# Kernel tuning notes

Measured on AMD Instinct MI355X. Metric: run time of the kernel, lower is better.

Reference implementation:

```python
import jax, jax.numpy as jnp
import numpy as np

K = 3
PAD = 1

def conv2d(x, w, b=None):
    # x: [B,C,H,W], w: [O,C,kh,kw], stride 1, padding 1
    y = jax.lax.conv_general_dilated(x, w, (1, 1), [(PAD, PAD), (PAD, PAD)],
                                     dimension_numbers=('NCHW', 'OIHW', 'NCHW'))
    if b is not None:
        y = y + b[None, :, None, None]
    return y

def deform_conv2d(x, offset, mask, w):
    # Faithful torchvision DeformConv2d (v2, stride=1, dilation=1, pad=1, no bias).
    # x: [B,C,H,W]; offset: [B,2*K*K,H,W] with (dy,dx) interleaved per kernel pt;
    # mask: [B,K*K,H,W]; w: [O,C,K,K]
    B, C, H, W = x.shape
    KK = K * K
    off = offset.reshape(B, KK, 2, H, W)
    offs_y, offs_x = off[:, :, 0], off[:, :, 1]           # [B,KK,H,W]
    ky = (jnp.arange(KK) // K).astype(jnp.float32) - PAD   # kernel row offsets
    kx = (jnp.arange(KK) % K).astype(jnp.float32) - PAD    # kernel col offsets
    py = offs_y + jnp.arange(H, dtype=jnp.float32)[None, None, :, None] + ky[None, :, None, None]
    px = offs_x + jnp.arange(W, dtype=jnp.float32)[None, None, None, :] + kx[None, :, None, None]
    y0f = jnp.floor(py); x0f = jnp.floor(px)
    wy = py - y0f; wx = px - x0f                           # bilinear fractions
    y0 = y0f.astype(jnp.int32); x0 = x0f.astype(jnp.int32)
    xf = x.reshape(B, C, H * W)

    def corner(yi, xi):
        valid = ((yi >= 0) & (yi < H) & (xi >= 0) & (xi < W)).astype(x.dtype)
        idx = jnp.clip(yi, 0, H - 1) * W + jnp.clip(xi, 0, W - 1)   # [B,KK,H,W]
        g = jax.vmap(lambda img, ix: img[:, ix])(xf, idx.reshape(B, KK * H * W))
        return g.reshape(B, C, KK, H, W) * valid[:, None]

    one = jnp.asarray(1.0, x.dtype)
    samp = (corner(y0, x0)         * ((one - wy) * (one - wx))[:, None]
          + corner(y0, x0 + 1)     * ((one - wy) * wx)[:, None]
          + corner(y0 + 1, x0)     * (wy * (one - wx))[:, None]
          + corner(y0 + 1, x0 + 1) * (wy * wx)[:, None])       # [B,C,KK,H,W]
    if mask is not None:
        samp = samp * mask[:, None]
    O = w.shape[0]
    return jnp.einsum('bckhw,ock->bohw', samp, w.reshape(O, C, KK))

def setup_inputs() -> dict:
    key = jax.random.key(0)
    ks = jax.random.split(key, 7)
    B, C, O, H, W = 4, 64, 64, 128, 128
    x = jax.random.normal(ks[0], (B, C, H, W), jnp.float32)
    ele = jax.random.normal(ks[1], (B, 1, H, W), jnp.float32)
    offset_w = jax.random.normal(ks[2], (2 * K * K, 1, 3, 3), jnp.float32) * 0.1
    offset_b = jnp.zeros((2 * K * K,), jnp.float32)
    mask_w = jax.random.normal(ks[3], (K * K, C, 3, 3), jnp.float32) * (1.0 / np.sqrt(C * 9))
    mask_b = jnp.zeros((K * K,), jnp.float32)
    deform_w = jax.random.normal(ks[4], (O, C, K, K), jnp.float32) * (1.0 / np.sqrt(C * 9))
    return {"x": x, "ele": ele, "offset_w": offset_w, "offset_b": offset_b,
            "mask_w": mask_w, "mask_b": mask_b, "deform_w": deform_w}

def reference(x, ele, offset_w, offset_b, mask_w, mask_b, deform_w):
    offset = conv2d(ele, offset_w, offset_b)                 # [B,18,H,W]
    mask = jax.nn.sigmoid(conv2d(x, mask_w, mask_b))         # [B,9,H,W]
    out = deform_conv2d(x, offset, mask, deform_w)           # [B,O,H,W]
    return jax.nn.relu(out)
```

## Files before the change

kernel.cpp:

```cpp
#include <hip/hip_runtime.h>
#include <hip/hip_bf16.h>
#include <hip/hip_fp16.h>

typedef _Float16 half8 __attribute__((ext_vector_type(8)));
typedef _Float16 half2v __attribute__((ext_vector_type(2)));
typedef float f32x4 __attribute__((ext_vector_type(4)));

#define B_ 4
#define C_ 64
#define O_ 64
#define H_ 128
#define W_ 128
#define HT 8
#define WT 16
#define HALO 3
#define RS 14
#define CS 22

__device__ __forceinline__ unsigned pkh(float lo, float hi) {
  half2v v = {(_Float16)lo, (_Float16)hi};
  return __builtin_bit_cast(unsigned, v);
}

__global__ void build_frags(const float* __restrict__ dw,
                            const float* __restrict__ mw,
                            _Float16* __restrict__ wsb) {
  int t = blockIdx.x * 256 + threadIdx.x;
  if (t < 36864) {
    int j = t & 7, lane = (t >> 3) & 63, ot = (t >> 9) & 3, s = t >> 11;
    int kk = s >> 1, ch = s & 1;
    int o = ot * 16 + (lane & 15);
    int c = ch * 32 + ((lane >> 4) << 3) + j;
    wsb[t] = (_Float16)dw[(o * 64 + c) * 9 + kk];
  } else if (t < 46080) {
    int t2 = t - 36864;
    int j = t2 & 7, lane = (t2 >> 3) & 63, s = t2 >> 9;
    int km = lane & 15;
    int c = (s & 1) * 32 + ((lane >> 4) << 3) + j;
    int tap = s >> 1;
    float v = (km < 9) ? mw[(km * 64 + c) * 9 + tap] : 0.0f;
    wsb[t] = (_Float16)v;
  }
}

__global__ __launch_bounds__(512, 4)
void deform_main(const float* __restrict__ x,
                 const float* __restrict__ ele,
                 const float* __restrict__ ow,
                 const float* __restrict__ ob,
                 const float* __restrict__ mb,
                 const _Float16* __restrict__ wsb,
                 float* __restrict__ out) {
  __shared__ uint4 xs4[RS * CS * 9];
  __shared__ _Float16 offl[128 * 18];
  __shared__ uint2 cwb[128 * 9];
  __shared__ unsigned crc[128 * 9];

  const int tid = threadIdx.x;
  const int lane = tid & 63;
  const int wv = tid >> 6;
  const int pcl = lane & 15;
  const int lq = lane >> 4;

  const int bid = blockIdx.x;
  const int d = ((bid & 7) << 6) + (bid >> 3);
  const int b = d >> 7;
  const int t7 = d & 127;
  const int r0 = (t7 >> 3) * HT;
  const int c0 = (t7 & 7) * WT;

  float ev[9];
  {
    int tl = tid & 127;
    int pr = tl >> 4, pc = tl & 15;
    int h = r0 + pr, w = c0 + pc;
#pragma unroll
    for (int ty = 0; ty < 3; ++ty)
#pragma unroll
      for (int tx = 0; tx < 3; ++tx) {
        int gy = h - 1 + ty, gx = w - 1 + tx;
        float v = 0.0f;
        if ((unsigned)gy < 128u && (unsigned)gx < 128u)
          v = ele[b * (H_ * W_) + (gy << 7) + gx];
        ev[ty * 3 + tx] = v;
      }
  }

  {
    _Float16* xsb = (_Float16*)xs4;
    const int c2 = tid >> 4;
    const int pl = tid & 15;
    const float* xb0 = x + b * (C_ * H_ * W_) + (2 * c2) * (H_ * W_);
    const float* xb1 = xb0 + (H_ * W_);
    for (int p = pl; p < RS * CS; p += 16) {
      int row = (p * 2979) >> 16;
      int col = p - row * CS;
      int gy = r0 - HALO + row, gx = c0 - HALO + col;
      float v0 = 0.0f, v1 = 0.0f;
      if ((unsigned)gy < 128u && (unsigned)gx < 128u) {
        int gi = (gy << 7) + gx;
        v0 = xb0[gi];
        v1 = xb1[gi];
      }
      half2v hv = {(_Float16)v0, (_Float16)v1};
      *(half2v*)&xsb[p * 72 + 2 * c2] = hv;
    }
  }

  if (tid < 128) {
#pragma unroll
    for (int ci = 0; ci < 18; ++ci) {
      float a = ob[ci];
#pragma unroll
      for (int tap = 0; tap < 9; ++tap) a += ev[tap] * ow[ci * 9 + tap];
      offl[tid * 18 + ci] = (_Float16)a;
    }
  }
  __syncthreads();

  {
    const half8* wfm8 = ((const half8*)wsb) + 4608;
    f32x4 macc = {0.f, 0.f, 0.f, 0.f};
#pragma unroll
    for (int s = 0; s < 18; ++s) {
      const int tap = s >> 1;
      const int chalf = s & 1;
      const int ty = tap / 3, tx = tap - ty * 3;
      half8 aw = wfm8[s * 64 + lane];
      const int csl = chalf * 4 + lq;
      int rc = (wv + (HALO - 1) + ty) * CS + (pcl + (HALO - 1) + tx);
      half8 xv = *(const half8*)(xs4 + rc * 9 + csl);
      macc = __builtin_amdgcn_mfma_f32_16x16x32_f16(aw, xv, macc, 0, 0, 0);
    }
    const int px = wv * 16 + pcl;
    const int h = r0 + wv, w = c0 + pcl;
#pragma unroll
    for (int r = 0; r < 4; ++r) {
      int kk = lq * 4 + r;
      if (kk < 9) {
        float a = macc[r] + mb[kk];
        float m = 1.0f / (1.0f + __expf(-a));
        int ky = kk / 3 - 1;
        int kx = kk - (kk / 3) * 3 - 1;
        half2v o2 = *(const half2v*)&offl[px * 18 + kk * 2];
        float py = (float)(h + ky) + (float)o2[0];
        float pxx = (float)(w + kx) + (float)o2[1];
        float fy = floorf(py), fx = floorf(pxx);
        float wy = py - fy, wx = pxx - fx;
        int iy = (int)fy - r0 + HALO;
        int ix = (int)fx - c0 + HALO;
        int vy0 = (unsigned)iy < (unsigned)RS;
        int vy1 = (unsigned)(iy + 1) < (unsigned)RS;
        int vx0 = (unsigned)ix < (unsigned)CS;
        int vx1 = (unsigned)(ix + 1) < (unsigned)CS;
        int cy0 = min(max(iy, 0), RS - 1), cy1 = min(max(iy + 1, 0), RS - 1);
        int cx0 = min(max(ix, 0), CS - 1), cx1 = min(max(ix + 1, 0), CS - 1);
        float wy0 = 1.0f - wy, wx0 = 1.0f - wx;
        float a00 = wy0 * wx0 * m * (float)(vy0 & vx0);
        float a01 = wy0 * wx * m * (float)(vy0 & vx1);
        float a10 = wy * wx0 * m * (float)(vy1 & vx0);
        float a11 = wy * wx * m * (float)(vy1 & vx1);
        int rc00 = cy0 * CS + cx0;
        int drow = (cy1 - cy0) * CS;
        int dcol = cx1 - cx0;
        uint2 cv;
        cv.x = pkh(a00, a01);
        cv.y = pkh(a10, a11);
        cwb[px * 9 + kk] = cv;
        crc[px * 9 + kk] =
            (unsigned)rc00 | ((unsigned)drow << 16) | ((unsigned)dcol << 24);
      }
    }
  }
  __syncthreads();

  const half8* wf8 = (const half8*)wsb;
  f32x4 acc[4];
#pragma unroll
  for (int ot = 0; ot < 4; ++ot) {
    f32x4 z = {0.f, 0.f, 0.f, 0.f};
    acc[ot] = z;
  }

  const int px = wv * 16 + pcl;

#pragma unroll
  for (int kk = 0; kk < 9; ++kk) {
    uint2 cv = cwb[px * 9 + kk];
    unsigned rv = crc[px * 9 + kk];
    int rc00 = rv & 0xFFFF;
    int drow = (rv >> 16) & 0xFF;
    int dcol = rv >> 24;
    int rc01 = rc00 + dcol;
    int rc10 = rc00 + drow;
    int rc11 = rc10 + dcol;
    half2v c01 = __builtin_bit_cast(half2v, cv.x);
    half2v c23 = __builtin_bit_cast(half2v, cv.y);
    _Float16 a00 = c01[0], a01 = c01[1], a10 = c23[0], a11 = c23[1];
    half8 a00s = {a00, a00, a00, a00, a00, a00, a00, a00};
    half8 a01s = {a01, a01, a01, a01, a01, a01, a01, a01};
    half8 a10s = {a10, a10, a10, a10, a10, a10, a10, a10};
    half8 a11s = {a11, a11, a11, a11, a11, a11, a11, a11};
#pragma unroll
    for (int ch = 0; ch < 2; ++ch) {
      const int csl = ch * 4 + lq;
      half8 v00 = *(const half8*)(xs4 + rc00 * 9 + csl);
      half8 v01 = *(const half8*)(xs4 + rc01 * 9 + csl);
      half8 v10 = *(const half8*)(xs4 + rc10 * 9 + csl);
      half8 v11 = *(const half8*)(xs4 + rc11 * 9 + csl);
      half8 t = v00 * a00s + v01 * a01s + v10 * a10s + v11 * a11s;
      const int sidx = kk * 2 + ch;
#pragma unroll
      for (int ot = 0; ot < 4; ++ot) {
        half8 bw = wf8[(sidx * 4 + ot) * 64 + lane];
        acc[ot] = __builtin_amdgcn_mfma_f32_16x16x32_f16(bw, t, acc[ot], 0, 0, 0);
      }
    }
  }

  const int h = r0 + wv;
  const int w = c0 + pcl;
#pragma unroll
  for (int ot = 0; ot < 4; ++ot) {
#pragma unroll
    for (int r = 0; r < 4; ++r) {
      int o = ot * 16 + lq * 4 + r;
      float v = fmaxf(acc[ot][r], 0.0f);
      out[((b * O_ + o) << 14) + (h << 7) + w] = v;
    }
  }
}

extern "C" void kernel_launch(void* const* d_in, const int* in_sizes, int n_in,
                              void* d_out, int out_size, void* d_ws, size_t ws_size,
                              hipStream_t stream) {
  const float* x   = (const float*)d_in[0];
  const float* ele = (const float*)d_in[1];
  const float* ow  = (const float*)d_in[2];
  const float* ob  = (const float*)d_in[3];
  const float* mw  = (const float*)d_in[4];
  const float* mb  = (const float*)d_in[5];
  const float* dw  = (const float*)d_in[6];
  _Float16* wsb = (_Float16*)d_ws;

  build_frags<<<180, 256, 0, stream>>>(dw, mw, wsb);
  deform_main<<<512, 512, 0, stream>>>(x, ele, ow, ob, mb, wsb,
                                       (float*)d_out);
}
```

Before: 32.17 us.

## Split deform MFMA reduction across wave halves with two pixel tiles per wave

Each wave now handles 32 pixels (two 16-pixel tiles) over half of the 18 kernel-tap/channel steps. Each weight fragment loaded from global memory therefore feeds two MFMAs, halving weight-fragment loads per pixel. The two K-halves are combined through a shared-memory reduction buffer that aliases the offset/coefficient scratch. This costs extra barriers, shared-memory traffic and more accumulator registers, and only half the waves do the final stores.

```diff
diff --git a/kernel.cpp b/kernel.cpp
--- a/kernel.cpp
+++ b/kernel.cpp
@@ -52,9 +52,11 @@
                  const _Float16* __restrict__ wsb,
                  float* __restrict__ out) {
   __shared__ uint4 xs4[RS * CS * 9];
-  __shared__ _Float16 offl[128 * 18];
-  __shared__ uint2 cwb[128 * 9];
-  __shared__ unsigned crc[128 * 9];
+  __shared__ uint4 dynbuf4[1152];
+  _Float16* offl = (_Float16*)dynbuf4;
+  uint2* cwb = (uint2*)((char*)dynbuf4 + 4608);
+  unsigned* crc = (unsigned*)((char*)dynbuf4 + 4608 + 9216);
+  f32x4* redbuf = (f32x4*)dynbuf4;
 
   const int tid = threadIdx.x;
   const int lane = tid & 63;
@@ -175,59 +177,85 @@
   __syncthreads();
 
   const half8* wf8 = (const half8*)wsb;
-  f32x4 acc[4];
-#pragma unroll
-  for (int ot = 0; ot < 4; ++ot) {
-    f32x4 z = {0.f, 0.f, 0.f, 0.f};
-    acc[ot] = z;
-  }
-
-  const int px = wv * 16 + pcl;
-
-#pragma unroll
-  for (int kk = 0; kk < 9; ++kk) {
-    uint2 cv = cwb[px * 9 + kk];
-    unsigned rv = crc[px * 9 + kk];
-    int rc00 = rv & 0xFFFF;
-    int drow = (rv >> 16) & 0xFF;
-    int dcol = rv >> 24;
-    int rc01 = rc00 + dcol;
-    int rc10 = rc00 + drow;
-    int rc11 = rc10 + dcol;
-    half2v c01 = __builtin_bit_cast(half2v, cv.x);
-    half2v c23 = __builtin_bit_cast(half2v, cv.y);
-    _Float16 a00 = c01[0], a01 = c01[1], a10 = c23[0], a11 = c23[1];
-    half8 a00s = {a00, a00, a00, a00, a00, a00, a00, a00};
-    half8 a01s = {a01, a01, a01, a01, a01, a01, a01, a01};
-    half8 a10s = {a10, a10, a10, a10, a10, a10, a10, a10};
-    half8 a11s = {a11, a11, a11, a11, a11, a11, a11, a11};
-#pragma unroll
-    for (int ch = 0; ch < 2; ++ch) {
-      const int csl = ch * 4 + lq;
+  const int pxg = wv & 3;
+  const int kh = wv >> 2;
+  f32x4 acc[2][4];
+#pragma unroll
+  for (int pt = 0; pt < 2; ++pt)
+#pragma unroll
+    for (int ot = 0; ot < 4; ++ot) {
+      f32x4 z = {0.f, 0.f, 0.f, 0.f};
+      acc[pt][ot] = z;
+    }
+
+  const int pxA = pxg * 32 + pcl;
+  const int pxB = pxA + 16;
+
+#pragma unroll
+  for (int s = 0; s < 9; ++s) {
+    const int sidx = kh * 9 + s;
+    const int kk = sidx >> 1;
+    const int ch = sidx & 1;
+    const int csl = ch * 4 + lq;
+    half8 t[2];
+#pragma unroll
+    for (int pt = 0; pt < 2; ++pt) {
+      const int px = pt ? pxB : pxA;
+      uint2 cv = cwb[px * 9 + kk];
+      unsigned rv = crc[px * 9 + kk];
+      int rc00 = rv & 0xFFFF;
+      int drow = (rv >> 16) & 0xFF;
+      int dcol = rv >> 24;
+      int rc01 = rc00 + dcol;
+      int rc10 = rc00 + drow;
+      int rc11 = rc10 + dcol;
+      half2v c01 = __builtin_bit_cast(half2v, cv.x);
+      half2v c23 = __builtin_bit_cast(half2v, cv.y);
+      _Float16 a00 = c01[0], a01 = c01[1], a10 = c23[0], a11 = c23[1];
+      half8 a00s = {a00, a00, a00, a00, a00, a00, a00, a00};
+      half8 a01s = {a01, a01, a01, a01, a01, a01, a01, a01};
+      half8 a10s = {a10, a10, a10, a10, a10, a10, a10, a10};
+      half8 a11s = {a11, a11, a11, a11, a11, a11, a11, a11};
       half8 v00 = *(const half8*)(xs4 + rc00 * 9 + csl);
       half8 v01 = *(const half8*)(xs4 + rc01 * 9 + csl);
       half8 v10 = *(const half8*)(xs4 + rc10 * 9 + csl);
       half8 v11 = *(const half8*)(xs4 + rc11 * 9 + csl);
-      half8 t = v00 * a00s + v01 * a01s + v10 * a10s + v11 * a11s;
-      const int sidx = kk * 2 + ch;
+      t[pt] = v00 * a00s + v01 * a01s + v10 * a10s + v11 * a11s;
+    }
+#pragma unroll
+    for (int ot = 0; ot < 4; ++ot) {
+      half8 bw = wf8[(sidx * 4 + ot) * 64 + lane];
+      acc[0][ot] = __builtin_amdgcn_mfma_f32_16x16x32_f16(bw, t[0], acc[0][ot], 0, 0, 0);
+      acc[1][ot] = __builtin_amdgcn_mfma_f32_16x16x32_f16(bw, t[1], acc[1][ot], 0, 0, 0);
+    }
+  }
+
+  __syncthreads();
+
+#pragma unroll
+  for (int pt = 0; pt < 2; ++pt) {
+    if (kh == 1) {
+#pragma unroll
+      for (int ot = 0; ot < 4; ++ot)
+        redbuf[((pxg * 4 + ot) * 4 + lq) * 16 + pcl] = acc[pt][ot];
+    }
+    __syncthreads();
+    if (kh == 0) {
+      const int px = pt ? pxB : pxA;
+      const int h = r0 + (px >> 4);
+      const int w = c0 + pcl;
 #pragma unroll
       for (int ot = 0; ot < 4; ++ot) {
-        half8 bw = wf8[(sidx * 4 + ot) * 64 + lane];
-        acc[ot] = __builtin_amdgcn_mfma_f32_16x16x32_f16(bw, t, acc[ot], 0, 0, 0);
-      }
-    }
-  }
-
-  const int h = r0 + wv;
-  const int w = c0 + pcl;
-#pragma unroll
-  for (int ot = 0; ot < 4; ++ot) {
-#pragma unroll
-    for (int r = 0; r < 4; ++r) {
-      int o = ot * 16 + lq * 4 + r;
-      float v = fmaxf(acc[ot][r], 0.0f);
-      out[((b * O_ + o) << 14) + (h << 7) + w] = v;
-    }
+        f32x4 other = redbuf[((pxg * 4 + ot) * 4 + lq) * 16 + pcl];
+#pragma unroll
+        for (int r = 0; r < 4; ++r) {
+          int o = ot * 16 + lq * 4 + r;
+          float v = fmaxf(acc[pt][ot][r] + other[r], 0.0f);
+          out[((b * O_ + o) << 14) + (h << 7) + w] = v;
+        }
+      }
+    }
+    __syncthreads();
   }
 }
 
```

Measured after the change: 31.22 us. 1.03x faster.
